# Kernel optimization log

Hardware: AMD Instinct MI355X
Metric: run time of the kernel (lower is better)

## Reference

```python
import jax, jax.numpy as jnp
import numpy as np

# Grid / model dims
B, H, W = 1, 90, 180
P = H * W                 # 16200 spatial points
MODEL_DIM = 130
L = MODEL_DIM - 2         # learnable_dim = 128
NH, HD = 8, 16            # n_heads, head_dim
S = 16                    # shared_hidden (DISCO out_channels)
K = 25                    # number of DISCO basis functions (piecewise-linear 5x5)
NNB = 25                  # neighbors per output point (theta_cutoff stencil)
MH = 32                   # head MLP hidden
FH = 256                  # FFN hidden


def setup_inputs() -> dict:
    key = jax.random.key(0)
    ks = jax.random.split(key, 12)
    x = jax.random.normal(ks[0], (B, H, W, MODEL_DIM), dtype=jnp.float32)
    # sparse DISCO structure: neighbor indices + precomputed (quadrature-weighted) basis values
    nbr_idx = jax.random.randint(ks[1], (P, NNB), 0, P, dtype=jnp.int32)
    basis_vals = jax.random.normal(ks[2], (K, P, NNB), dtype=jnp.float32) * 0.1
    # learnable DISCO kernel weights (out_channels=S, in_channels=1, K basis coeffs) + bias
    disco_w = jax.random.normal(ks[3], (S, K), dtype=jnp.float32) / np.sqrt(K).astype(np.float32)
    disco_b = jax.random.normal(ks[4], (S,), dtype=jnp.float32) * 0.01
    # per-head MLP params: S -> MH -> 1, one set per head
    head_w1 = jax.random.normal(ks[5], (NH, S, MH), dtype=jnp.float32) / np.sqrt(S).astype(np.float32)
    head_b1 = jnp.zeros((NH, MH), dtype=jnp.float32)
    head_w2 = jax.random.normal(ks[6], (NH, MH, 1), dtype=jnp.float32) / np.sqrt(MH).astype(np.float32)
    head_b2 = jnp.zeros((NH, 1), dtype=jnp.float32)
    # FFN: model_dim -> FH -> L, with the sin/cos input columns zeroed (as in __init__)
    ffn_w1 = jax.random.normal(ks[7], (MODEL_DIM, FH), dtype=jnp.float32) / np.sqrt(MODEL_DIM).astype(np.float32)
    ffn_w1 = ffn_w1.at[-2:, :].set(0.0)
    ffn_b1 = jnp.zeros((FH,), dtype=jnp.float32)
    ffn_w2 = jax.random.normal(ks[8], (FH, L), dtype=jnp.float32) / np.sqrt(FH).astype(np.float32)
    ffn_b2 = jnp.zeros((L,), dtype=jnp.float32)
    return dict(x=x, nbr_idx=nbr_idx, basis_vals=basis_vals, disco_w=disco_w, disco_b=disco_b,
                head_w1=head_w1, head_b1=head_b1, head_w2=head_w2, head_b2=head_b2,
                ffn_w1=ffn_w1, ffn_b1=ffn_b1, ffn_w2=ffn_w2, ffn_b2=ffn_b2)


def reference(x, nbr_idx, basis_vals, disco_w, disco_b,
              head_w1, head_b1, head_w2, head_b2,
              ffn_w1, ffn_b1, ffn_w2, ffn_b2):
    gelu = lambda t: jax.nn.gelu(t, approximate=False)  # torch nn.GELU default is exact
    x_learn = x[..., :L]          # (B,H,W,L)
    sin_cos = x[..., L:]          # (B,H,W,2)
    x_res = x_learn

    # ---- DISCO spherical conv, depthwise over B*L channels (in_channels=1) ----
    xf = jnp.transpose(x_learn, (0, 3, 1, 2)).reshape(B * L, P)      # (N, P)
    gathered = xf[:, nbr_idx]                                        # (N, P, NNB) irregular gather
    z = jnp.einsum('kpn,cpn->ckp', basis_vals, gathered)             # (N, K, P) basis projections
    y = jnp.einsum('sk,ckp->csp', disco_w, z) + disco_b[None, :, None]  # (N, S, P)
    disco_out = y.reshape(B, L, S, H, W).transpose(0, 3, 4, 1, 2)    # (B,H,W,L,S)

    # ---- per-head MLP, vectorized over heads ----
    hfeat = disco_out.reshape(B, H, W, NH, HD, S)                    # (B,H,W,NH,HD,S)
    h1 = gelu(jnp.einsum('bxyhds,hsm->bxyhdm', hfeat, head_w1) + head_b1[:, None, :])
    hout = jnp.einsum('bxyhdm,hmo->bxyhdo', h1, head_w2) + head_b2[:, None, :]  # o=1
    x_mix = hout.reshape(B, H, W, L)                                 # heads concatenated in order
    x_mix = x_mix + x_res                                            # residual

    # ---- FFN channel mixing on [x_mix, sin_cos] ----
    x_full = jnp.concatenate([x_mix, sin_cos], axis=-1)              # (B,H,W,MODEL_DIM)
    hf = gelu(jnp.einsum('bxyd,df->bxyf', x_full, ffn_w1) + ffn_b1)
    x_ffn = jnp.einsum('bxyf,fl->bxyl', hf, ffn_w2) + ffn_b2
    x_out = x_ffn + x_mix
    return jnp.concatenate([x_out, sin_cos], axis=-1)                # (B,H,W,MODEL_DIM)
```

## Files before the change

### kernel.cpp

```cpp
#include <hip/hip_runtime.h>
#include <hip/hip_bf16.h>

#define P_TOT 16200
#define MODEL_DIMC 130
#define L_DIM 128
#define NHH 8
#define HDD 16
#define S_DIM 16
#define K_DIM 25
#define NNBC 25
#define MH_DIM 32
#define FH_DIM 256

__device__ __forceinline__ float gelu_f(float x) {
    float z = fabsf(x) * 0.70710678118654752440f;
    float t = __fdividef(1.0f, fmaf(0.3275911f, z, 1.0f));
    float poly = t * fmaf(t, fmaf(t, fmaf(t, fmaf(t, 1.061405429f, -1.453152027f),
                                          1.421413741f), -0.284496736f), 0.254829592f);
    float e = __expf(-z * z);
    float erfp = fmaf(-poly, e, 1.0f);
    float erfv = copysignf(erfp, x);
    return 0.5f * x * (1.0f + erfv);
}

__global__ __launch_bounds__(256) void k1_bw(const float* __restrict__ basis,
                                             const float* __restrict__ disco_w,
                                             float* __restrict__ bw) {
    __shared__ float w[S_DIM * K_DIM];
    int tid = threadIdx.x;
    for (int i = tid; i < S_DIM * K_DIM; i += 256) w[i] = disco_w[i];
    __syncthreads();
    int i = blockIdx.x * 256 + tid;
    if (i >= P_TOT * NNBC) return;
    float bv[K_DIM];
#pragma unroll
    for (int k = 0; k < K_DIM; k++) bv[k] = basis[k * (P_TOT * NNBC) + i];
    float acc[S_DIM];
#pragma unroll
    for (int s = 0; s < S_DIM; s++) {
        float a = 0.f;
#pragma unroll
        for (int k = 0; k < K_DIM; k++) a = fmaf(w[s * K_DIM + k], bv[k], a);
        acc[s] = a;
    }
    float4* outp = (float4*)(bw + (size_t)i * S_DIM);
#pragma unroll
    for (int q = 0; q < 4; q++) {
        float4 v; v.x = acc[q*4+0]; v.y = acc[q*4+1]; v.z = acc[q*4+2]; v.w = acc[q*4+3];
        outp[q] = v;
    }
}

__global__ __launch_bounds__(256) void k2_disco_head(
        const float* __restrict__ x, const int* __restrict__ nbr,
        const float* __restrict__ bw,
        const float* __restrict__ head_w1, const float* __restrict__ head_b1,
        const float* __restrict__ head_w2, const float* __restrict__ head_b2,
        const float* __restrict__ disco_b,
        float* __restrict__ xmix) {
    __shared__ __align__(16) float w1t[NHH * 516];
    __shared__ float b1s[NHH * 33];
    __shared__ float w2s[NHH * 33];
    __shared__ float b2s[NHH];
    __shared__ float dbs[S_DIM];
    __shared__ __align__(16) float bws[4][NNBC * S_DIM];
    __shared__ int nbrs[4][NNBC];

    int tid = threadIdx.x;
    for (int i = tid; i < NHH * S_DIM * MH_DIM; i += 256) {
        int h = i >> 9, s = (i >> 5) & 15, m = i & 31;
        w1t[h * 516 + m * 16 + s] = head_w1[i];
    }
    for (int i = tid; i < NHH * MH_DIM; i += 256) {
        int h = i >> 5, m = i & 31;
        b1s[h * 33 + m] = head_b1[i];
        w2s[h * 33 + m] = head_w2[i];
    }
    if (tid < NHH) b2s[tid] = head_b2[tid];
    if (tid < S_DIM) dbs[tid] = disco_b[tid];

    int wv = tid >> 6, lane = tid & 63;
    int p = blockIdx.x * 4 + wv;
    if (lane < NNBC) nbrs[wv][lane] = nbr[p * NNBC + lane];
    {
        const float4* src = (const float4*)(bw + (size_t)p * (NNBC * S_DIM));
        float4* dst = (float4*)bws[wv];
        for (int j = lane; j < (NNBC * S_DIM) / 4; j += 64) dst[j] = src[j];
    }
    __syncthreads();

    float y0[16], y1[16];
#pragma unroll
    for (int s = 0; s < 16; s++) { y0[s] = dbs[s]; y1[s] = dbs[s]; }

    const float* xb0 = x + lane;
    const float* xb1 = x + 64 + lane;
#pragma unroll 5
    for (int n = 0; n < NNBC; n++) {
        int u = nbrs[wv][n];
        float g0 = xb0[u * MODEL_DIMC];
        float g1 = xb1[u * MODEL_DIMC];
        const float4* bwn = (const float4*)&bws[wv][n * 16];
#pragma unroll
        for (int q = 0; q < 4; q++) {
            float4 b4 = bwn[q];
            y0[q*4+0] = fmaf(g0, b4.x, y0[q*4+0]);
            y0[q*4+1] = fmaf(g0, b4.y, y0[q*4+1]);
            y0[q*4+2] = fmaf(g0, b4.z, y0[q*4+2]);
            y0[q*4+3] = fmaf(g0, b4.w, y0[q*4+3]);
            y1[q*4+0] = fmaf(g1, b4.x, y1[q*4+0]);
            y1[q*4+1] = fmaf(g1, b4.y, y1[q*4+1]);
            y1[q*4+2] = fmaf(g1, b4.z, y1[q*4+2]);
            y1[q*4+3] = fmaf(g1, b4.w, y1[q*4+3]);
        }
    }

    int h0 = lane >> 4, h1 = h0 + 4;
    float acc0 = b2s[h0], acc1 = b2s[h1];
    const float* w1t0 = &w1t[h0 * 516];
    const float* w1t1 = &w1t[h1 * 516];
#pragma unroll 8
    for (int m = 0; m < MH_DIM; m++) {
        float a0 = b1s[h0 * 33 + m], a1 = b1s[h1 * 33 + m];
        const float4* r0 = (const float4*)&w1t0[m * 16];
        const float4* r1 = (const float4*)&w1t1[m * 16];
#pragma unroll
        for (int q = 0; q < 4; q++) {
            float4 wa = r0[q];
            a0 = fmaf(y0[q*4+0], wa.x, a0);
            a0 = fmaf(y0[q*4+1], wa.y, a0);
            a0 = fmaf(y0[q*4+2], wa.z, a0);
            a0 = fmaf(y0[q*4+3], wa.w, a0);
            float4 wb = r1[q];
            a1 = fmaf(y1[q*4+0], wb.x, a1);
            a1 = fmaf(y1[q*4+1], wb.y, a1);
            a1 = fmaf(y1[q*4+2], wb.z, a1);
            a1 = fmaf(y1[q*4+3], wb.w, a1);
        }
        a0 = gelu_f(a0);
        a1 = gelu_f(a1);
        acc0 = fmaf(a0, w2s[h0 * 33 + m], acc0);
        acc1 = fmaf(a1, w2s[h1 * 33 + m], acc1);
    }
    float xm0 = acc0 + x[p * MODEL_DIMC + lane];
    float xm1 = acc1 + x[p * MODEL_DIMC + 64 + lane];
    xmix[p * L_DIM + lane] = xm0;
    xmix[p * L_DIM + 64 + lane] = xm1;
}

__global__ __launch_bounds__(256) void k3_ffn(
        const float* __restrict__ x, const float* __restrict__ xmix,
        const float* __restrict__ w1, const float* __restrict__ b1,
        const float* __restrict__ w2, const float* __restrict__ b2,
        float* __restrict__ out) {
    __shared__ __align__(16) float xm[32 * 128];
    __shared__ __align__(16) float hf[32 * 260];
    int tid = threadIdx.x;
    int p0 = blockIdx.x * 32;
    int valid = min(32, P_TOT - p0);
    {
        int nf4 = (valid * 128) / 4;
        const float4* src = (const float4*)(xmix + (size_t)p0 * 128);
        float4* dst = (float4*)xm;
        for (int j = tid; j < nf4; j += 256) dst[j] = src[j];
    }
    __syncthreads();

    int fg = tid & 31, pg = tid >> 5;
    float acc[4][8];
#pragma unroll
    for (int i = 0; i < 4; i++)
#pragma unroll
        for (int j = 0; j < 8; j++) acc[i][j] = b1[fg * 8 + j];

#pragma unroll 4
    for (int k = 0; k < 128; k++) {
        float4 wA = *(const float4*)&w1[k * FH_DIM + fg * 8];
        float4 wB = *(const float4*)&w1[k * FH_DIM + fg * 8 + 4];
#pragma unroll
        for (int i = 0; i < 4; i++) {
            float xv = xm[(pg * 4 + i) * 128 + k];
            acc[i][0] = fmaf(xv, wA.x, acc[i][0]);
            acc[i][1] = fmaf(xv, wA.y, acc[i][1]);
            acc[i][2] = fmaf(xv, wA.z, acc[i][2]);
            acc[i][3] = fmaf(xv, wA.w, acc[i][3]);
            acc[i][4] = fmaf(xv, wB.x, acc[i][4]);
            acc[i][5] = fmaf(xv, wB.y, acc[i][5]);
            acc[i][6] = fmaf(xv, wB.z, acc[i][6]);
            acc[i][7] = fmaf(xv, wB.w, acc[i][7]);
        }
    }
#pragma unroll
    for (int i = 0; i < 4; i++) {
        int pl = pg * 4 + i;
#pragma unroll
        for (int j = 0; j < 8; j++) hf[pl * 260 + fg * 8 + j] = gelu_f(acc[i][j]);
    }
    __syncthreads();

    int lg = tid & 31;
    float acc2[4][4];
#pragma unroll
    for (int i = 0; i < 4; i++)
#pragma unroll
        for (int j = 0; j < 4; j++) acc2[i][j] = b2[lg * 4 + j];

#pragma unroll 4
    for (int f = 0; f < FH_DIM; f++) {
        float4 wv = *(const float4*)&w2[f * L_DIM + lg * 4];
#pragma unroll
        for (int i = 0; i < 4; i++) {
            float hv = hf[(pg * 4 + i) * 260 + f];
            acc2[i][0] = fmaf(hv, wv.x, acc2[i][0]);
            acc2[i][1] = fmaf(hv, wv.y, acc2[i][1]);
            acc2[i][2] = fmaf(hv, wv.z, acc2[i][2]);
            acc2[i][3] = fmaf(hv, wv.w, acc2[i][3]);
        }
    }
#pragma unroll
    for (int i = 0; i < 4; i++) {
        int pl = pg * 4 + i;
        if (pl < valid) {
            int p = p0 + pl;
            float2 o01, o23;
            o01.x = acc2[i][0] + xm[pl * 128 + lg * 4 + 0];
            o01.y = acc2[i][1] + xm[pl * 128 + lg * 4 + 1];
            o23.x = acc2[i][2] + xm[pl * 128 + lg * 4 + 2];
            o23.y = acc2[i][3] + xm[pl * 128 + lg * 4 + 3];
            *(float2*)&out[p * MODEL_DIMC + lg * 4 + 0] = o01;
            *(float2*)&out[p * MODEL_DIMC + lg * 4 + 2] = o23;
            if (lg == 0) {
                float2 sc;
                sc.x = x[p * MODEL_DIMC + 128];
                sc.y = x[p * MODEL_DIMC + 129];
                *(float2*)&out[p * MODEL_DIMC + 128] = sc;
            }
        }
    }
}

extern "C" void kernel_launch(void* const* d_in, const int* in_sizes, int n_in,
                              void* d_out, int out_size, void* d_ws, size_t ws_size,
                              hipStream_t stream) {
    const float* x        = (const float*)d_in[0];
    const int*   nbr      = (const int*)  d_in[1];
    const float* basis    = (const float*)d_in[2];
    const float* disco_w  = (const float*)d_in[3];
    const float* disco_b  = (const float*)d_in[4];
    const float* head_w1  = (const float*)d_in[5];
    const float* head_b1  = (const float*)d_in[6];
    const float* head_w2  = (const float*)d_in[7];
    const float* head_b2  = (const float*)d_in[8];
    const float* ffn_w1   = (const float*)d_in[9];
    const float* ffn_b1   = (const float*)d_in[10];
    const float* ffn_w2   = (const float*)d_in[11];
    const float* ffn_b2   = (const float*)d_in[12];
    float* out = (float*)d_out;

    float* bw   = (float*)d_ws;
    float* xmix = bw + (size_t)P_TOT * NNBC * S_DIM;

    hipLaunchKernelGGL(k1_bw, dim3((P_TOT * NNBC + 255) / 256), dim3(256), 0, stream,
                       basis, disco_w, bw);
    hipLaunchKernelGGL(k2_disco_head, dim3(P_TOT / 4), dim3(256), 0, stream,
                       x, nbr, bw, head_w1, head_b1, head_w2, head_b2, disco_b, xmix);
    hipLaunchKernelGGL(k3_ffn, dim3((P_TOT + 31) / 32), dim3(256), 0, stream,
                       x, xmix, ffn_w1, ffn_b1, ffn_w2, ffn_b2, out);
}
```

Measured before the change: 277.9 us.

## Split k2 channels across two waves per point and batch neighbor gathers

The disco/head kernel now gives each point two wavefronts, one per 64-channel half. Before, one wavefront handled both halves with two accumulator sets. This halves per-thread registers and raises occupancy. Each block now covers 2 points, so the grid doubles and the per-block load of head weights into shared memory is repeated twice as often. Gathers are grouped five neighbors at a time to expose memory-level parallelism, and the GELU reciprocal uses the hardware rcp builtin.

```diff
diff --git a/kernel.cpp b/kernel.cpp
--- a/kernel.cpp
+++ b/kernel.cpp
@@ -14,7 +14,7 @@
 
 __device__ __forceinline__ float gelu_f(float x) {
     float z = fabsf(x) * 0.70710678118654752440f;
-    float t = __fdividef(1.0f, fmaf(0.3275911f, z, 1.0f));
+    float t = __builtin_amdgcn_rcpf(fmaf(0.3275911f, z, 1.0f));
     float poly = t * fmaf(t, fmaf(t, fmaf(t, fmaf(t, 1.061405429f, -1.453152027f),
                                           1.421413741f), -0.284496736f), 0.254829592f);
     float e = __expf(-z * z);
@@ -63,8 +63,8 @@
     __shared__ float w2s[NHH * 33];
     __shared__ float b2s[NHH];
     __shared__ float dbs[S_DIM];
-    __shared__ __align__(16) float bws[4][NNBC * S_DIM];
-    __shared__ int nbrs[4][NNBC];
+    __shared__ __align__(16) float bws[2][NNBC * S_DIM];
+    __shared__ int nbrs[2][NNBC];
 
     int tid = threadIdx.x;
     for (int i = tid; i < NHH * S_DIM * MH_DIM; i += 256) {
@@ -79,73 +79,68 @@
     if (tid < NHH) b2s[tid] = head_b2[tid];
     if (tid < S_DIM) dbs[tid] = disco_b[tid];
 
+    int p0 = blockIdx.x * 2;
+    {
+        const float4* src = (const float4*)(bw + (size_t)p0 * (NNBC * S_DIM));
+        float4* dst = (float4*)&bws[0][0];
+        for (int j = tid; j < (2 * NNBC * S_DIM) / 4; j += 256) dst[j] = src[j];
+    }
+    if (tid < 2 * NNBC) nbrs[0][tid] = nbr[p0 * NNBC + tid];
+    __syncthreads();
+
     int wv = tid >> 6, lane = tid & 63;
-    int p = blockIdx.x * 4 + wv;
-    if (lane < NNBC) nbrs[wv][lane] = nbr[p * NNBC + lane];
-    {
-        const float4* src = (const float4*)(bw + (size_t)p * (NNBC * S_DIM));
-        float4* dst = (float4*)bws[wv];
-        for (int j = lane; j < (NNBC * S_DIM) / 4; j += 64) dst[j] = src[j];
-    }
-    __syncthreads();
-
-    float y0[16], y1[16];
-#pragma unroll
-    for (int s = 0; s < 16; s++) { y0[s] = dbs[s]; y1[s] = dbs[s]; }
-
-    const float* xb0 = x + lane;
-    const float* xb1 = x + 64 + lane;
+    int ptl = wv >> 1;
+    int c = (wv & 1) * 64 + lane;
+    int p = p0 + ptl;
+
+    float y[16];
+#pragma unroll
+    for (int s = 0; s < 16; s++) y[s] = dbs[s];
+
+    const float* xb = x + c;
 #pragma unroll 5
-    for (int n = 0; n < NNBC; n++) {
-        int u = nbrs[wv][n];
-        float g0 = xb0[u * MODEL_DIMC];
-        float g1 = xb1[u * MODEL_DIMC];
-        const float4* bwn = (const float4*)&bws[wv][n * 16];
+    for (int nb = 0; nb < NNBC; nb += 5) {
+        float g[5];
+#pragma unroll
+        for (int j = 0; j < 5; j++) {
+            int u = nbrs[ptl][nb + j];
+            g[j] = xb[(size_t)u * MODEL_DIMC];
+        }
+#pragma unroll
+        for (int j = 0; j < 5; j++) {
+            const float4* bwn = (const float4*)&bws[ptl][(nb + j) * 16];
+#pragma unroll
+            for (int q = 0; q < 4; q++) {
+                float4 b4 = bwn[q];
+                y[q*4+0] = fmaf(g[j], b4.x, y[q*4+0]);
+                y[q*4+1] = fmaf(g[j], b4.y, y[q*4+1]);
+                y[q*4+2] = fmaf(g[j], b4.z, y[q*4+2]);
+                y[q*4+3] = fmaf(g[j], b4.w, y[q*4+3]);
+            }
+        }
+    }
+
+    int h = c >> 4;
+    float acc = b2s[h];
+    const float* wrow = &w1t[h * 516];
+    const float* b1r  = &b1s[h * 33];
+    const float* w2r  = &w2s[h * 33];
+#pragma unroll 4
+    for (int m = 0; m < MH_DIM; m++) {
+        float a = b1r[m];
+        const float4* r = (const float4*)&wrow[m * 16];
 #pragma unroll
         for (int q = 0; q < 4; q++) {
-            float4 b4 = bwn[q];
-            y0[q*4+0] = fmaf(g0, b4.x, y0[q*4+0]);
-            y0[q*4+1] = fmaf(g0, b4.y, y0[q*4+1]);
-            y0[q*4+2] = fmaf(g0, b4.z, y0[q*4+2]);
-            y0[q*4+3] = fmaf(g0, b4.w, y0[q*4+3]);
-            y1[q*4+0] = fmaf(g1, b4.x, y1[q*4+0]);
-            y1[q*4+1] = fmaf(g1, b4.y, y1[q*4+1]);
-            y1[q*4+2] = fmaf(g1, b4.z, y1[q*4+2]);
-            y1[q*4+3] = fmaf(g1, b4.w, y1[q*4+3]);
-        }
-    }
-
-    int h0 = lane >> 4, h1 = h0 + 4;
-    float acc0 = b2s[h0], acc1 = b2s[h1];
-    const float* w1t0 = &w1t[h0 * 516];
-    const float* w1t1 = &w1t[h1 * 516];
-#pragma unroll 8
-    for (int m = 0; m < MH_DIM; m++) {
-        float a0 = b1s[h0 * 33 + m], a1 = b1s[h1 * 33 + m];
-        const float4* r0 = (const float4*)&w1t0[m * 16];
-        const float4* r1 = (const float4*)&w1t1[m * 16];
-#pragma unroll
-        for (int q = 0; q < 4; q++) {
-            float4 wa = r0[q];
-            a0 = fmaf(y0[q*4+0], wa.x, a0);
-            a0 = fmaf(y0[q*4+1], wa.y, a0);
-            a0 = fmaf(y0[q*4+2], wa.z, a0);
-            a0 = fmaf(y0[q*4+3], wa.w, a0);
-            float4 wb = r1[q];
-            a1 = fmaf(y1[q*4+0], wb.x, a1);
-            a1 = fmaf(y1[q*4+1], wb.y, a1);
-            a1 = fmaf(y1[q*4+2], wb.z, a1);
-            a1 = fmaf(y1[q*4+3], wb.w, a1);
-        }
-        a0 = gelu_f(a0);
-        a1 = gelu_f(a1);
-        acc0 = fmaf(a0, w2s[h0 * 33 + m], acc0);
-        acc1 = fmaf(a1, w2s[h1 * 33 + m], acc1);
-    }
-    float xm0 = acc0 + x[p * MODEL_DIMC + lane];
-    float xm1 = acc1 + x[p * MODEL_DIMC + 64 + lane];
-    xmix[p * L_DIM + lane] = xm0;
-    xmix[p * L_DIM + 64 + lane] = xm1;
+            float4 wa = r[q];
+            a = fmaf(y[q*4+0], wa.x, a);
+            a = fmaf(y[q*4+1], wa.y, a);
+            a = fmaf(y[q*4+2], wa.z, a);
+            a = fmaf(y[q*4+3], wa.w, a);
+        }
+        a = gelu_f(a);
+        acc = fmaf(a, w2r[m], acc);
+    }
+    xmix[p * L_DIM + c] = acc + x[(size_t)p * MODEL_DIMC + c];
 }
 
 __global__ __launch_bounds__(256) void k3_ffn(
@@ -262,7 +257,7 @@
 
     hipLaunchKernelGGL(k1_bw, dim3((P_TOT * NNBC + 255) / 256), dim3(256), 0, stream,
                        basis, disco_w, bw);
-    hipLaunchKernelGGL(k2_disco_head, dim3(P_TOT / 4), dim3(256), 0, stream,
+    hipLaunchKernelGGL(k2_disco_head, dim3(P_TOT / 2), dim3(256), 0, stream,
                        x, nbr, bw, head_w1, head_b1, head_w2, head_b2, disco_b, xmix);
     hipLaunchKernelGGL(k3_ffn, dim3((P_TOT + 31) / 32), dim3(256), 0, stream,
                        x, xmix, ffn_w1, ffn_b1, ffn_w2, ffn_b2, out);
```

After: 259.7 us. -6.6%, faster.
